# Performance work log

Measured on AMD Instinct MI355X. Metric: run time of the kernel, lower is better.

The kernel has to match this reference:

```python
import jax, jax.numpy as jnp
import numpy as np

N = 300_000   # octree nodes at this depth
K = 27        # 3x3x3 deconv kernel taps
CIN = 32
COUT = 32
G = 8         # group norm groups
B = 8         # octrees in batch
EPS = 1e-5


def setup_inputs() -> dict:
    key = jax.random.key(0)
    k1, k2, k3, k4 = jax.random.split(key, 4)
    data = jax.random.normal(k1, (N, CIN), jnp.float32)
    neigh = jax.random.randint(k2, (N, K), 0, N, jnp.int32)          # neighbor index table
    batch_id = jnp.sort(jax.random.randint(k3, (N,), 0, B, jnp.int32))  # sorted per-node octree id
    weights = jax.random.normal(k4, (K, CIN, COUT), jnp.float32) * 0.05
    gamma = jnp.ones((COUT,), jnp.float32)
    beta = jnp.zeros((COUT,), jnp.float32)
    return dict(data=data, weights=weights, gamma=gamma, beta=beta,
                neigh=neigh, batch_id=batch_id, n_batch=B)


def _octree_group_norm(h, batch_id, gamma, beta, n_batch):
    # Per-octree (segment) group norm, following ocnn.OctreeGroupNorm:
    # count = n_nodes_per_octree * C/G; inv_count = 1/(count+eps);
    # per-group mean/var via scatter_add then within-group channel sum.
    Nn, C = h.shape
    Cg = C // G
    cnt = jax.ops.segment_sum(jnp.ones((Nn,), h.dtype), batch_id,
                              num_segments=n_batch) * (C / G)   # [B]
    inv_cnt = 1.0 / (cnt + EPS)
    s = jax.ops.segment_sum(h, batch_id, num_segments=n_batch)   # [B, C]
    mean_g = s.reshape(n_batch, G, Cg).sum(-1) * inv_cnt[:, None]  # [B, G]
    mean = jnp.repeat(mean_g, Cg, axis=1)                          # [B, C]
    hc = h - mean[batch_id]
    v = jax.ops.segment_sum(hc * hc, batch_id, num_segments=n_batch)
    var_g = v.reshape(n_batch, G, Cg).sum(-1) * inv_cnt[:, None]
    inv_std = jnp.repeat(1.0 / jnp.sqrt(var_g + EPS), Cg, axis=1)  # [B, C]
    return hc * inv_std[batch_id] * gamma + beta


def reference(data, weights, gamma, beta, neigh, batch_id, n_batch):
    # Octree deconv (stride=1): gather 27 neighbors, small matmul per tap, sum.
    x = data[neigh]                                # [N, K, Cin] irregular gather
    out = jnp.einsum('nki,kio->no', x, weights)    # [N, Cout]
    out = _octree_group_norm(out, batch_id, gamma, beta, n_batch)
    return jax.nn.relu(out)
```

## Files before the change

kernel.cpp:

```cpp
#include <hip/hip_runtime.h>
#include <math.h>

#define EPS 1e-5f

typedef __attribute__((ext_vector_type(8)))  _Float16 half8;
typedef __attribute__((ext_vector_type(16))) float    floatx16;

__device__ __forceinline__ unsigned short f2h_bits(float f) {
    _Float16 h = (_Float16)f;
    return __builtin_bit_cast(unsigned short, h);
}

__global__ __launch_bounds__(256) void pack_all_kernel(
    const float* __restrict__ data, unsigned short* __restrict__ dpk,
    const float* __restrict__ W, unsigned short* __restrict__ wpk,
    const int* __restrict__ neigh, int* __restrict__ neighp,
    float* __restrict__ gzero, int N, int nbData)
{
    const int b = blockIdx.x;
    const int tid = threadIdx.x;

    if (b < nbData) {
        const int i = b * 256 + tid;
        if (i >= N * 8) return;
        const float4 v = ((const float4*)data)[i];
        ushort4 o;
        o.x = f2h_bits(v.x);
        o.y = f2h_bits(v.y);
        o.z = f2h_bits(v.z);
        o.w = f2h_bits(v.w);
        ((ushort4*)dpk)[i] = o;
        return;
    }
    const int wb = b - nbData;
    if (wb < 14) {
        const int t = wb * 256 + tid;
        const int l = t & 63;
        const int c = (t >> 6) & 1;
        const int k = t >> 7;
        ushort4 o0 = make_ushort4(0, 0, 0, 0), o1 = o0;
        if (k < 27) {
            const int n  = l & 31;
            const int cb = c * 16 + (l >> 5) * 8;
            const float* wp = W + k * 1024 + n;
            o0.x = f2h_bits(wp[(cb + 0) * 32]);
            o0.y = f2h_bits(wp[(cb + 1) * 32]);
            o0.z = f2h_bits(wp[(cb + 2) * 32]);
            o0.w = f2h_bits(wp[(cb + 3) * 32]);
            o1.x = f2h_bits(wp[(cb + 4) * 32]);
            o1.y = f2h_bits(wp[(cb + 5) * 32]);
            o1.z = f2h_bits(wp[(cb + 6) * 32]);
            o1.w = f2h_bits(wp[(cb + 7) * 32]);
        }
        *(ushort4*)(wpk + (size_t)t * 8)     = o0;
        *(ushort4*)(wpk + (size_t)t * 8 + 4) = o1;
        return;
    }
    if (wb == 14) {
        if (tid < 520) gzero[tid] = 0.f;
        return;
    }
    const int i = (wb - 15) * 256 + tid;
    if (i >= N * 28) return;
    const int n = i / 28;
    const int k = i % 28;
    neighp[i] = neigh[n * 27 + (k < 27 ? k : 26)];
}

__global__ __launch_bounds__(512, 4) void deconv_stats_kernel(
    const unsigned short* __restrict__ dpk, const unsigned short* __restrict__ wpk,
    const int* __restrict__ nbase, int nstride, int quadok,
    const int* __restrict__ batch_id, float* __restrict__ out,
    float* __restrict__ gs1, float* __restrict__ gs2, float* __restrict__ gcnt,
    int N)
{
    __shared__ unsigned short BW[28 * 2 * 64 * 8];
    __shared__ float ls1[256];
    __shared__ float ls2[256];
    __shared__ float lcnt[8];

    const int t    = threadIdx.x;
    const int wv   = t >> 6;
    const int l    = t & 63;
    const int mrow = l & 31;
    const int half = l >> 5;
    const int wbase = blockIdx.x * 256 + wv * 32;
    const int node  = wbase + mrow;
    const int nc    = node < N ? node : N - 1;

#pragma unroll
    for (int r = 0; r < 7; ++r)
        ((int4*)BW)[r * 512 + t] = ((const int4*)wpk)[r * 512 + t];
    if (t < 256) {
        ls1[t] = 0.f;
        ls2[t] = 0.f;
    }
    if (t < 8) lcnt[t] = 0.f;
    __syncthreads();

    floatx16 acc;
#pragma unroll
    for (int r = 0; r < 16; ++r) acc[r] = 0.f;

    const int* nrow = nbase + (size_t)nc * nstride;
    const int aoff  = half * 8;

    int4 nq;
    if (quadok) nq = ((const int4*)nrow)[0];
    else { nq.x = nrow[0]; nq.y = nrow[1]; nq.z = nrow[2]; nq.w = nrow[3]; }

    half8 a0, a1, a2, a3, a4, a5, a6, a7;
    {
        const unsigned short* r0 = dpk + (size_t)nq.x * 32;
        const unsigned short* r1 = dpk + (size_t)nq.y * 32;
        const unsigned short* r2 = dpk + (size_t)nq.z * 32;
        const unsigned short* r3 = dpk + (size_t)nq.w * 32;
        a0 = *(const half8*)(r0 + aoff);  a1 = *(const half8*)(r0 + 16 + aoff);
        a2 = *(const half8*)(r1 + aoff);  a3 = *(const half8*)(r1 + 16 + aoff);
        a4 = *(const half8*)(r2 + aoff);  a5 = *(const half8*)(r2 + 16 + aoff);
        a6 = *(const half8*)(r3 + aoff);  a7 = *(const half8*)(r3 + 16 + aoff);
    }

    const half8* BL = (const half8*)BW;

#pragma unroll 1
    for (int it = 0; it < 7; ++it) {
        half8 b0, b1, b2, b3, b4, b5, b6, b7;
        if (it < 6) {
            int4 nqn;
            if (quadok) nqn = ((const int4*)nrow)[it + 1];
            else {
                const int kb = (it + 1) * 4;
                nqn.x = nrow[kb];
                nqn.y = nrow[kb + 1];
                nqn.z = nrow[kb + 2];
                nqn.w = nrow[kb + 3 < 27 ? kb + 3 : 26];
            }
            const unsigned short* r0 = dpk + (size_t)nqn.x * 32;
            const unsigned short* r1 = dpk + (size_t)nqn.y * 32;
            const unsigned short* r2 = dpk + (size_t)nqn.z * 32;
            const unsigned short* r3 = dpk + (size_t)nqn.w * 32;
            b0 = *(const half8*)(r0 + aoff);  b1 = *(const half8*)(r0 + 16 + aoff);
            b2 = *(const half8*)(r1 + aoff);  b3 = *(const half8*)(r1 + 16 + aoff);
            b4 = *(const half8*)(r2 + aoff);  b5 = *(const half8*)(r2 + 16 + aoff);
            b6 = *(const half8*)(r3 + aoff);  b7 = *(const half8*)(r3 + 16 + aoff);
        }

        acc = __builtin_amdgcn_mfma_f32_32x32x16_f16(a0, BL[(8 * it + 0) * 64 + l], acc, 0, 0, 0);
        acc = __builtin_amdgcn_mfma_f32_32x32x16_f16(a1, BL[(8 * it + 1) * 64 + l], acc, 0, 0, 0);
        acc = __builtin_amdgcn_mfma_f32_32x32x16_f16(a2, BL[(8 * it + 2) * 64 + l], acc, 0, 0, 0);
        acc = __builtin_amdgcn_mfma_f32_32x32x16_f16(a3, BL[(8 * it + 3) * 64 + l], acc, 0, 0, 0);
        acc = __builtin_amdgcn_mfma_f32_32x32x16_f16(a4, BL[(8 * it + 4) * 64 + l], acc, 0, 0, 0);
        acc = __builtin_amdgcn_mfma_f32_32x32x16_f16(a5, BL[(8 * it + 5) * 64 + l], acc, 0, 0, 0);
        acc = __builtin_amdgcn_mfma_f32_32x32x16_f16(a6, BL[(8 * it + 6) * 64 + l], acc, 0, 0, 0);
        acc = __builtin_amdgcn_mfma_f32_32x32x16_f16(a7, BL[(8 * it + 7) * 64 + l], acc, 0, 0, 0);

        if (it < 6) {
            a0 = b0; a1 = b1; a2 = b2; a3 = b3;
            a4 = b4; a5 = b5; a6 = b6; a7 = b7;
        }
    }

    const int co = mrow;
#pragma unroll
    for (int r = 0; r < 16; ++r) {
        const int row = (r & 3) + 8 * (r >> 2) + 4 * half;
        const int n = wbase + row;
        if (n < N) out[(size_t)n * 32 + co] = acc[r];
    }

    bool fast = (wbase + 31 < N);
    int bfst = 0;
    if (fast) {
        bfst = batch_id[wbase];
        fast = (bfst == batch_id[wbase + 31]);
    }
    if (fast) {
        float s1 = 0.f, s2 = 0.f;
#pragma unroll
        for (int r = 0; r < 16; ++r) {
            const float v = acc[r];
            s1 += v;
            s2 += v * v;
        }
        atomicAdd(&ls1[bfst * 32 + co], s1);
        atomicAdd(&ls2[bfst * 32 + co], s2);
    } else {
#pragma unroll
        for (int r = 0; r < 16; ++r) {
            const int row = (r & 3) + 8 * (r >> 2) + 4 * half;
            const int n = wbase + row;
            if (n < N) {
                const int b = batch_id[n];
                const float v = acc[r];
                atomicAdd(&ls1[b * 32 + co], v);
                atomicAdd(&ls2[b * 32 + co], v * v);
            }
        }
    }
    if (half == 0) {
        const int n = wbase + mrow;
        if (n < N) atomicAdd(&lcnt[batch_id[n]], 1.0f);
    }
    __syncthreads();

    if (t < 256) {
        float v;
        v = ls1[t]; if (v != 0.f) atomicAdd(&gs1[t], v);
        v = ls2[t]; if (v != 0.f) atomicAdd(&gs2[t], v);
        if (t < 8) { v = lcnt[t]; if (v != 0.f) atomicAdd(&gcnt[t], v); }
    }
}

__global__ __launch_bounds__(256) void gn_relu_kernel(
    float* __restrict__ out, const int* __restrict__ batch_id,
    const float* __restrict__ gs1, const float* __restrict__ gs2,
    const float* __restrict__ gcnt, const float* __restrict__ gamma,
    const float* __restrict__ beta, int N)
{
    const int idx = blockIdx.x * 256 + threadIdx.x;
    if (idx >= N * 8) return;
    const int n = idx >> 3;
    const int g = idx & 7;
    const int b = batch_id[n];

    const float cnt  = gcnt[b] * 4.0f;
    const float icnt = 1.0f / (cnt + EPS);
    const float4 s1 = *(const float4*)(gs1 + b * 32 + g * 4);
    const float4 s2 = *(const float4*)(gs2 + b * 32 + g * 4);
    const float S1 = s1.x + s1.y + s1.z + s1.w;
    const float S2 = s2.x + s2.y + s2.z + s2.w;
    const float m   = S1 * icnt;
    const float var = (S2 - 2.0f * m * S1 + cnt * m * m) * icnt;
    const float istd = rsqrtf(var + EPS);

    const float4 gm4 = *(const float4*)(gamma + g * 4);
    const float4 bt4 = *(const float4*)(beta + g * 4);
    float4 h = *(float4*)(out + (size_t)idx * 4);
    h.x = fmaxf((h.x - m) * istd * gm4.x + bt4.x, 0.f);
    h.y = fmaxf((h.y - m) * istd * gm4.y + bt4.y, 0.f);
    h.z = fmaxf((h.z - m) * istd * gm4.z + bt4.z, 0.f);
    h.w = fmaxf((h.w - m) * istd * gm4.w + bt4.w, 0.f);
    *(float4*)(out + (size_t)idx * 4) = h;
}

extern "C" void kernel_launch(void* const* d_in, const int* in_sizes, int n_in,
                              void* d_out, int out_size, void* d_ws, size_t ws_size,
                              hipStream_t stream) {
    const float* data     = (const float*)d_in[0];
    const float* weights  = (const float*)d_in[1];
    const float* gamma    = (const float*)d_in[2];
    const float* beta     = (const float*)d_in[3];
    const int*   neigh    = (const int*)d_in[4];
    const int*   batch_id = (const int*)d_in[5];
    const int N = in_sizes[0] / 32;
    float* out = (float*)d_out;

    char* wsb = (char*)d_ws;
    float* gs1  = (float*)wsb;
    float* gs2  = gs1 + 256;
    float* gcnt = gs1 + 512;
    unsigned short* dpk = (unsigned short*)(wsb + 4096);
    unsigned short* wpk = (unsigned short*)(wsb + 4096 + (size_t)N * 64);
    int* neighp = (int*)(wsb + 4096 + (size_t)N * 64 + 57344);

    const size_t need = 4096 + (size_t)N * 64 + 57344 + (size_t)N * 112;
    const int pack_ok = (ws_size >= need) ? 1 : 0;

    const int nbData  = (N * 8 + 255) / 256;
    const int nbNeigh = pack_ok ? (N * 28 + 255) / 256 : 0;
    hipLaunchKernelGGL(pack_all_kernel, dim3(nbData + 15 + nbNeigh), dim3(256),
                       0, stream, data, dpk, weights, wpk, neigh, neighp,
                       gs1, N, nbData);

    const int* nbase  = pack_ok ? neighp : neigh;
    const int nstride = pack_ok ? 28 : 27;

    const int nblocks = (N + 255) / 256;
    hipLaunchKernelGGL(deconv_stats_kernel, dim3(nblocks), dim3(512), 0, stream,
                       dpk, wpk, nbase, nstride, pack_ok, batch_id, out,
                       gs1, gs2, gcnt, N);

    const int n8 = N * 8;
    hipLaunchKernelGGL(gn_relu_kernel, dim3((n8 + 255) / 256), dim3(256), 0,
                       stream, out, batch_id, gs1, gs2, gcnt, gamma, beta, N);
}
```

Measured before the change: 287.1 us.

## Partition gather source into slices so each pass hits a cache-resident window

The deconv kernel now makes four passes over all 27 taps. In each pass only neighbours whose index falls in the current quarter of the node range are gathered; all others are redirected to a zeroed padding row at index N, which is added to the packed data buffer. The aim is to keep the gathered working set of each pass small enough to stay in cache, at the cost of issuing four times as many MFMAs and gather instructions. Neighbour indices are loaded once into registers with nontemporal loads, and output stores become nontemporal.

```diff
diff --git a/kernel.cpp b/kernel.cpp
--- a/kernel.cpp
+++ b/kernel.cpp
@@ -2,9 +2,11 @@
 #include <math.h>
 
 #define EPS 1e-5f
+#define NPASS 4
 
 typedef __attribute__((ext_vector_type(8)))  _Float16 half8;
 typedef __attribute__((ext_vector_type(16))) float    floatx16;
+typedef __attribute__((ext_vector_type(4)))  int      iv4;
 
 __device__ __forceinline__ unsigned short f2h_bits(float f) {
     _Float16 h = (_Float16)f;
@@ -58,6 +60,7 @@
     }
     if (wb == 14) {
         if (tid < 520) gzero[tid] = 0.f;
+        if (tid >= 192 && tid < 256) dpk[(size_t)N * 32 + (tid - 192)] = 0;
         return;
     }
     const int i = (wb - 15) * 256 + tid;
@@ -67,12 +70,36 @@
     neighp[i] = neigh[n * 27 + (k < 27 ? k : 26)];
 }
 
+#define EFFI(i) ((((unsigned)((i) - base)) < uss) ? (i) : N)
+
+#define LOADQ(d0,d1,d2,d3,d4,d5,d6,d7, nv) do {                              \
+    const unsigned short* r0 = dpk + (size_t)EFFI((nv).x) * 32;              \
+    const unsigned short* r1 = dpk + (size_t)EFFI((nv).y) * 32;              \
+    const unsigned short* r2 = dpk + (size_t)EFFI((nv).z) * 32;              \
+    const unsigned short* r3 = dpk + (size_t)EFFI((nv).w) * 32;              \
+    d0 = *(const half8*)(r0 + aoff);  d1 = *(const half8*)(r0 + 16 + aoff);  \
+    d2 = *(const half8*)(r1 + aoff);  d3 = *(const half8*)(r1 + 16 + aoff);  \
+    d4 = *(const half8*)(r2 + aoff);  d5 = *(const half8*)(r2 + 16 + aoff);  \
+    d6 = *(const half8*)(r3 + aoff);  d7 = *(const half8*)(r3 + 16 + aoff);  \
+} while (0)
+
+#define MFMAQ(iq, s0,s1,s2,s3,s4,s5,s6,s7) do {                              \
+    acc = __builtin_amdgcn_mfma_f32_32x32x16_f16(s0, BL[(8*(iq)+0)*64 + l], acc, 0, 0, 0); \
+    acc = __builtin_amdgcn_mfma_f32_32x32x16_f16(s1, BL[(8*(iq)+1)*64 + l], acc, 0, 0, 0); \
+    acc = __builtin_amdgcn_mfma_f32_32x32x16_f16(s2, BL[(8*(iq)+2)*64 + l], acc, 0, 0, 0); \
+    acc = __builtin_amdgcn_mfma_f32_32x32x16_f16(s3, BL[(8*(iq)+3)*64 + l], acc, 0, 0, 0); \
+    acc = __builtin_amdgcn_mfma_f32_32x32x16_f16(s4, BL[(8*(iq)+4)*64 + l], acc, 0, 0, 0); \
+    acc = __builtin_amdgcn_mfma_f32_32x32x16_f16(s5, BL[(8*(iq)+5)*64 + l], acc, 0, 0, 0); \
+    acc = __builtin_amdgcn_mfma_f32_32x32x16_f16(s6, BL[(8*(iq)+6)*64 + l], acc, 0, 0, 0); \
+    acc = __builtin_amdgcn_mfma_f32_32x32x16_f16(s7, BL[(8*(iq)+7)*64 + l], acc, 0, 0, 0); \
+} while (0)
+
 __global__ __launch_bounds__(512, 4) void deconv_stats_kernel(
     const unsigned short* __restrict__ dpk, const unsigned short* __restrict__ wpk,
     const int* __restrict__ nbase, int nstride, int quadok,
     const int* __restrict__ batch_id, float* __restrict__ out,
     float* __restrict__ gs1, float* __restrict__ gs2, float* __restrict__ gcnt,
-    int N)
+    int N, int slice_sz)
 {
     __shared__ unsigned short BW[28 * 2 * 64 * 8];
     __shared__ float ls1[256];
@@ -105,60 +132,48 @@
     const int* nrow = nbase + (size_t)nc * nstride;
     const int aoff  = half * 8;
 
-    int4 nq;
-    if (quadok) nq = ((const int4*)nrow)[0];
-    else { nq.x = nrow[0]; nq.y = nrow[1]; nq.z = nrow[2]; nq.w = nrow[3]; }
-
-    half8 a0, a1, a2, a3, a4, a5, a6, a7;
-    {
-        const unsigned short* r0 = dpk + (size_t)nq.x * 32;
-        const unsigned short* r1 = dpk + (size_t)nq.y * 32;
-        const unsigned short* r2 = dpk + (size_t)nq.z * 32;
-        const unsigned short* r3 = dpk + (size_t)nq.w * 32;
-        a0 = *(const half8*)(r0 + aoff);  a1 = *(const half8*)(r0 + 16 + aoff);
-        a2 = *(const half8*)(r1 + aoff);  a3 = *(const half8*)(r1 + 16 + aoff);
-        a4 = *(const half8*)(r2 + aoff);  a5 = *(const half8*)(r2 + 16 + aoff);
-        a6 = *(const half8*)(r3 + aoff);  a7 = *(const half8*)(r3 + 16 + aoff);
+    iv4 nq0, nq1, nq2, nq3, nq4, nq5, nq6;
+    if (quadok) {
+        const iv4* np = (const iv4*)nrow;
+        nq0 = __builtin_nontemporal_load(np + 0);
+        nq1 = __builtin_nontemporal_load(np + 1);
+        nq2 = __builtin_nontemporal_load(np + 2);
+        nq3 = __builtin_nontemporal_load(np + 3);
+        nq4 = __builtin_nontemporal_load(np + 4);
+        nq5 = __builtin_nontemporal_load(np + 5);
+        nq6 = __builtin_nontemporal_load(np + 6);
+    } else {
+        nq0 = (iv4){nrow[0],  nrow[1],  nrow[2],  nrow[3]};
+        nq1 = (iv4){nrow[4],  nrow[5],  nrow[6],  nrow[7]};
+        nq2 = (iv4){nrow[8],  nrow[9],  nrow[10], nrow[11]};
+        nq3 = (iv4){nrow[12], nrow[13], nrow[14], nrow[15]};
+        nq4 = (iv4){nrow[16], nrow[17], nrow[18], nrow[19]};
+        nq5 = (iv4){nrow[20], nrow[21], nrow[22], nrow[23]};
+        nq6 = (iv4){nrow[24], nrow[25], nrow[26], nrow[26]};
     }
 
     const half8* BL = (const half8*)BW;
+    const unsigned uss = (unsigned)slice_sz;
 
 #pragma unroll 1
-    for (int it = 0; it < 7; ++it) {
+    for (int p = 0; p < NPASS; ++p) {
+        const int base = p * slice_sz;
+        half8 a0, a1, a2, a3, a4, a5, a6, a7;
         half8 b0, b1, b2, b3, b4, b5, b6, b7;
-        if (it < 6) {
-            int4 nqn;
-            if (quadok) nqn = ((const int4*)nrow)[it + 1];
-            else {
-                const int kb = (it + 1) * 4;
-                nqn.x = nrow[kb];
-                nqn.y = nrow[kb + 1];
-                nqn.z = nrow[kb + 2];
-                nqn.w = nrow[kb + 3 < 27 ? kb + 3 : 26];
-            }
-            const unsigned short* r0 = dpk + (size_t)nqn.x * 32;
-            const unsigned short* r1 = dpk + (size_t)nqn.y * 32;
-            const unsigned short* r2 = dpk + (size_t)nqn.z * 32;
-            const unsigned short* r3 = dpk + (size_t)nqn.w * 32;
-            b0 = *(const half8*)(r0 + aoff);  b1 = *(const half8*)(r0 + 16 + aoff);
-            b2 = *(const half8*)(r1 + aoff);  b3 = *(const half8*)(r1 + 16 + aoff);
-            b4 = *(const half8*)(r2 + aoff);  b5 = *(const half8*)(r2 + 16 + aoff);
-            b6 = *(const half8*)(r3 + aoff);  b7 = *(const half8*)(r3 + 16 + aoff);
-        }
-
-        acc = __builtin_amdgcn_mfma_f32_32x32x16_f16(a0, BL[(8 * it + 0) * 64 + l], acc, 0, 0, 0);
-        acc = __builtin_amdgcn_mfma_f32_32x32x16_f16(a1, BL[(8 * it + 1) * 64 + l], acc, 0, 0, 0);
-        acc = __builtin_amdgcn_mfma_f32_32x32x16_f16(a2, BL[(8 * it + 2) * 64 + l], acc, 0, 0, 0);
-        acc = __builtin_amdgcn_mfma_f32_32x32x16_f16(a3, BL[(8 * it + 3) * 64 + l], acc, 0, 0, 0);
-        acc = __builtin_amdgcn_mfma_f32_32x32x16_f16(a4, BL[(8 * it + 4) * 64 + l], acc, 0, 0, 0);
-        acc = __builtin_amdgcn_mfma_f32_32x32x16_f16(a5, BL[(8 * it + 5) * 64 + l], acc, 0, 0, 0);
-        acc = __builtin_amdgcn_mfma_f32_32x32x16_f16(a6, BL[(8 * it + 6) * 64 + l], acc, 0, 0, 0);
-        acc = __builtin_amdgcn_mfma_f32_32x32x16_f16(a7, BL[(8 * it + 7) * 64 + l], acc, 0, 0, 0);
-
-        if (it < 6) {
-            a0 = b0; a1 = b1; a2 = b2; a3 = b3;
-            a4 = b4; a5 = b5; a6 = b6; a7 = b7;
-        }
+        LOADQ(a0,a1,a2,a3,a4,a5,a6,a7, nq0);
+        LOADQ(b0,b1,b2,b3,b4,b5,b6,b7, nq1);
+        MFMAQ(0, a0,a1,a2,a3,a4,a5,a6,a7);
+        LOADQ(a0,a1,a2,a3,a4,a5,a6,a7, nq2);
+        MFMAQ(1, b0,b1,b2,b3,b4,b5,b6,b7);
+        LOADQ(b0,b1,b2,b3,b4,b5,b6,b7, nq3);
+        MFMAQ(2, a0,a1,a2,a3,a4,a5,a6,a7);
+        LOADQ(a0,a1,a2,a3,a4,a5,a6,a7, nq4);
+        MFMAQ(3, b0,b1,b2,b3,b4,b5,b6,b7);
+        LOADQ(b0,b1,b2,b3,b4,b5,b6,b7, nq5);
+        MFMAQ(4, a0,a1,a2,a3,a4,a5,a6,a7);
+        LOADQ(a0,a1,a2,a3,a4,a5,a6,a7, nq6);
+        MFMAQ(5, b0,b1,b2,b3,b4,b5,b6,b7);
+        MFMAQ(6, a0,a1,a2,a3,a4,a5,a6,a7);
     }
 
     const int co = mrow;
@@ -166,7 +181,7 @@
     for (int r = 0; r < 16; ++r) {
         const int row = (r & 3) + 8 * (r >> 2) + 4 * half;
         const int n = wbase + row;
-        if (n < N) out[(size_t)n * 32 + co] = acc[r];
+        if (n < N) __builtin_nontemporal_store(acc[r], &out[(size_t)n * 32 + co]);
     }
 
     bool fast = (wbase + 31 < N);
@@ -260,11 +275,12 @@
     float* gs1  = (float*)wsb;
     float* gs2  = gs1 + 256;
     float* gcnt = gs1 + 512;
+    const size_t dpk_bytes = ((size_t)N + 2) * 64;
     unsigned short* dpk = (unsigned short*)(wsb + 4096);
-    unsigned short* wpk = (unsigned short*)(wsb + 4096 + (size_t)N * 64);
-    int* neighp = (int*)(wsb + 4096 + (size_t)N * 64 + 57344);
-
-    const size_t need = 4096 + (size_t)N * 64 + 57344 + (size_t)N * 112;
+    unsigned short* wpk = (unsigned short*)(wsb + 4096 + dpk_bytes);
+    int* neighp = (int*)(wsb + 4096 + dpk_bytes + 57344);
+
+    const size_t need = 4096 + dpk_bytes + 57344 + (size_t)N * 112;
     const int pack_ok = (ws_size >= need) ? 1 : 0;
 
     const int nbData  = (N * 8 + 255) / 256;
@@ -276,10 +292,11 @@
     const int* nbase  = pack_ok ? neighp : neigh;
     const int nstride = pack_ok ? 28 : 27;
 
+    const int slice_sz = (N + NPASS - 1) / NPASS;
     const int nblocks = (N + 255) / 256;
     hipLaunchKernelGGL(deconv_stats_kernel, dim3(nblocks), dim3(512), 0, stream,
                        dpk, wpk, nbase, nstride, pack_ok, batch_id, out,
-                       gs1, gs2, gcnt, N);
+                       gs1, gs2, gcnt, N, slice_sz);
 
     const int n8 = N * 8;
     hipLaunchKernelGGL(gn_relu_kernel, dim3((n8 + 255) / 256), dim3(256), 0,
```

New measurement: 574.4 us. 100% more time.

## Store pre-norm deconv output as fp16 intermediate and shrink deconv blocks to 256 threads

Applied to the files above, without the earlier changes.

The deconv kernel now writes its pre-normalization output as fp16 into a workspace buffer, and the group-norm/ReLU kernel reads it back and converts to float. This halves the intermediate write and read traffic between the two kernels. The deconv block also shrinks from 512 to 256 threads covering 128 nodes, which doubles the number of per-block weight staging loads into shared memory and may lower resident waves per CU. The fp16 rounding of pre-norm values adds a small precision loss.

```diff
diff --git a/kernel.cpp b/kernel.cpp
--- a/kernel.cpp
+++ b/kernel.cpp
@@ -67,10 +67,11 @@
     neighp[i] = neigh[n * 27 + (k < 27 ? k : 26)];
 }
 
-__global__ __launch_bounds__(512, 4) void deconv_stats_kernel(
+__global__ __launch_bounds__(256) void deconv_stats_kernel(
     const unsigned short* __restrict__ dpk, const unsigned short* __restrict__ wpk,
     const int* __restrict__ nbase, int nstride, int quadok,
     const int* __restrict__ batch_id, float* __restrict__ out,
+    unsigned short* __restrict__ hraw, int hok,
     float* __restrict__ gs1, float* __restrict__ gs2, float* __restrict__ gcnt,
     int N)
 {
@@ -84,17 +85,15 @@
     const int l    = t & 63;
     const int mrow = l & 31;
     const int half = l >> 5;
-    const int wbase = blockIdx.x * 256 + wv * 32;
+    const int wbase = blockIdx.x * 128 + wv * 32;
     const int node  = wbase + mrow;
     const int nc    = node < N ? node : N - 1;
 
 #pragma unroll
-    for (int r = 0; r < 7; ++r)
-        ((int4*)BW)[r * 512 + t] = ((const int4*)wpk)[r * 512 + t];
-    if (t < 256) {
-        ls1[t] = 0.f;
-        ls2[t] = 0.f;
-    }
+    for (int r = 0; r < 14; ++r)
+        ((int4*)BW)[r * 256 + t] = ((const int4*)wpk)[r * 256 + t];
+    ls1[t] = 0.f;
+    ls2[t] = 0.f;
     if (t < 8) lcnt[t] = 0.f;
     __syncthreads();
 
@@ -162,11 +161,20 @@
     }
 
     const int co = mrow;
-#pragma unroll
-    for (int r = 0; r < 16; ++r) {
-        const int row = (r & 3) + 8 * (r >> 2) + 4 * half;
-        const int n = wbase + row;
-        if (n < N) out[(size_t)n * 32 + co] = acc[r];
+    if (hok) {
+#pragma unroll
+        for (int r = 0; r < 16; ++r) {
+            const int row = (r & 3) + 8 * (r >> 2) + 4 * half;
+            const int n = wbase + row;
+            if (n < N) hraw[(size_t)n * 32 + co] = f2h_bits(acc[r]);
+        }
+    } else {
+#pragma unroll
+        for (int r = 0; r < 16; ++r) {
+            const int row = (r & 3) + 8 * (r >> 2) + 4 * half;
+            const int n = wbase + row;
+            if (n < N) out[(size_t)n * 32 + co] = acc[r];
+        }
     }
 
     bool fast = (wbase + 31 < N);
@@ -204,7 +212,7 @@
     }
     __syncthreads();
 
-    if (t < 256) {
+    {
         float v;
         v = ls1[t]; if (v != 0.f) atomicAdd(&gs1[t], v);
         v = ls2[t]; if (v != 0.f) atomicAdd(&gs2[t], v);
@@ -213,7 +221,8 @@
 }
 
 __global__ __launch_bounds__(256) void gn_relu_kernel(
-    float* __restrict__ out, const int* __restrict__ batch_id,
+    float* __restrict__ out, const unsigned short* __restrict__ hraw, int hok,
+    const int* __restrict__ batch_id,
     const float* __restrict__ gs1, const float* __restrict__ gs2,
     const float* __restrict__ gcnt, const float* __restrict__ gamma,
     const float* __restrict__ beta, int N)
@@ -236,7 +245,16 @@
 
     const float4 gm4 = *(const float4*)(gamma + g * 4);
     const float4 bt4 = *(const float4*)(beta + g * 4);
-    float4 h = *(float4*)(out + (size_t)idx * 4);
+    float4 h;
+    if (hok) {
+        const ushort4 hv = *(const ushort4*)(hraw + (size_t)idx * 4);
+        h.x = (float)__builtin_bit_cast(_Float16, hv.x);
+        h.y = (float)__builtin_bit_cast(_Float16, hv.y);
+        h.z = (float)__builtin_bit_cast(_Float16, hv.z);
+        h.w = (float)__builtin_bit_cast(_Float16, hv.w);
+    } else {
+        h = *(float4*)(out + (size_t)idx * 4);
+    }
     h.x = fmaxf((h.x - m) * istd * gm4.x + bt4.x, 0.f);
     h.y = fmaxf((h.y - m) * istd * gm4.y + bt4.y, 0.f);
     h.z = fmaxf((h.z - m) * istd * gm4.z + bt4.z, 0.f);
@@ -263,9 +281,13 @@
     unsigned short* dpk = (unsigned short*)(wsb + 4096);
     unsigned short* wpk = (unsigned short*)(wsb + 4096 + (size_t)N * 64);
     int* neighp = (int*)(wsb + 4096 + (size_t)N * 64 + 57344);
-
-    const size_t need = 4096 + (size_t)N * 64 + 57344 + (size_t)N * 112;
-    const int pack_ok = (ws_size >= need) ? 1 : 0;
+    unsigned short* hraw = (unsigned short*)(wsb + 4096 + (size_t)N * 64 + 57344
+                                             + (size_t)N * 112);
+
+    const size_t need_np = 4096 + (size_t)N * 64 + 57344 + (size_t)N * 112;
+    const size_t need_hr = need_np + (size_t)N * 64;
+    const int pack_ok = (ws_size >= need_np) ? 1 : 0;
+    const int hraw_ok = (ws_size >= need_hr) ? 1 : 0;
 
     const int nbData  = (N * 8 + 255) / 256;
     const int nbNeigh = pack_ok ? (N * 28 + 255) / 256 : 0;
@@ -276,12 +298,13 @@
     const int* nbase  = pack_ok ? neighp : neigh;
     const int nstride = pack_ok ? 28 : 27;
 
-    const int nblocks = (N + 255) / 256;
-    hipLaunchKernelGGL(deconv_stats_kernel, dim3(nblocks), dim3(512), 0, stream,
+    const int nblocks = (N + 127) / 128;
+    hipLaunchKernelGGL(deconv_stats_kernel, dim3(nblocks), dim3(256), 0, stream,
                        dpk, wpk, nbase, nstride, pack_ok, batch_id, out,
-                       gs1, gs2, gcnt, N);
+                       hraw, hraw_ok, gs1, gs2, gcnt, N);
 
     const int n8 = N * 8;
     hipLaunchKernelGGL(gn_relu_kernel, dim3((n8 + 255) / 256), dim3(256), 0,
-                       stream, out, batch_id, gs1, gs2, gcnt, gamma, beta, N);
-}
+                       stream, out, hraw, hraw_ok, batch_id,
+                       gs1, gs2, gcnt, gamma, beta, N);
+}
```

Measured after the change: 279.5 us. 1.03x faster.
